# Optimization experiments

Hardware: AMD Instinct MI355X
Metric: run time of the kernel (lower is better)

Reference implementation:

```python
import jax, jax.numpy as jnp
import numpy as np

N_NODES = 50000


def _gcn_conv(h, src, dst, W, b, n_nodes):
    """PyG GCNConv: add self-loops, symmetric deg^{-1/2} normalization,
    linear transform, scatter-add aggregation at target nodes."""
    h = h @ W  # [N, out]
    # self-loops
    loop = jnp.arange(n_nodes, dtype=src.dtype)
    s = jnp.concatenate([src, loop])  # source j
    d = jnp.concatenate([dst, loop])  # target i
    ones = jnp.ones(s.shape[0], dtype=h.dtype)
    deg = jax.ops.segment_sum(ones, d, num_segments=n_nodes)  # in-degree incl. self-loop
    dinv = jnp.where(deg > 0, jax.lax.rsqrt(deg), 0.0)
    norm = dinv[s] * dinv[d]  # [E+N]
    msg = h[s] * norm[:, None]  # gather + scale, [E+N, out]
    out = jax.ops.segment_sum(msg, d, num_segments=n_nodes)  # scatter-add
    return out + b


def reference(x, edge_index, q_emb, W1, b1, W2, b2, Wq, bq):
    src, dst = edge_index[0], edge_index[1]
    n = x.shape[0]
    # dropout rates are 0.0 -> identity
    h1 = jax.nn.relu(_gcn_conv(x, src, dst, W1, b1, n))
    h2 = _gcn_conv(h1, src, dst, W2, b2, n)
    ques = q_emb @ Wq + bq
    return (ques, h2)


def setup_inputs() -> dict:
    key = jax.random.key(0)
    ks = jax.random.split(key, 9)
    d = 128
    sc = 1.0 / np.sqrt(d)
    return {
        "x": jax.random.normal(ks[0], (N_NODES, d), dtype=jnp.float32),
        "edge_index": jax.random.randint(ks[1], (2, 800000), 0, N_NODES, dtype=jnp.int64),
        "q_emb": jax.random.normal(ks[2], (20000, d), dtype=jnp.float32),
        "W1": jax.random.normal(ks[3], (d, d), dtype=jnp.float32) * sc,
        "b1": jax.random.normal(ks[4], (d,), dtype=jnp.float32) * 0.01,
        "W2": jax.random.normal(ks[5], (d, d), dtype=jnp.float32) * sc,
        "b2": jax.random.normal(ks[6], (d,), dtype=jnp.float32) * 0.01,
        "Wq": jax.random.normal(ks[7], (d, d), dtype=jnp.float32) * sc,
        "bq": jax.random.normal(ks[8], (d,), dtype=jnp.float32) * 0.01,
    }
```

## Files before the change

### kernel.cpp

```cpp
#include <hip/hip_runtime.h>

#define D 128
#define NFB 768
#define CAP 64

typedef __attribute__((ext_vector_type(8))) short bf16x8;
typedef __attribute__((ext_vector_type(4))) float f32x4;

__device__ __forceinline__ unsigned short f2b(float v) {
    unsigned u = __float_as_uint(v);
    unsigned r = u + 0x7fffu + ((u >> 16) & 1u);
    return (unsigned short)(r >> 16);
}
__device__ __forceinline__ float b2f(unsigned short h) {
    return __uint_as_float(((unsigned)h) << 16);
}

__global__ __launch_bounds__(256) void fillw(const int* __restrict__ src,
                                             const int* __restrict__ dst,
                                             int* __restrict__ cnt,
                                             int* __restrict__ colv, int E,
                                             const float* __restrict__ W1,
                                             const float* __restrict__ W2,
                                             const float* __restrict__ Wq,
                                             unsigned short* __restrict__ o1,
                                             unsigned short* __restrict__ o2,
                                             unsigned short* __restrict__ oq) {
    int b = blockIdx.x;
    if (b >= NFB) {
        int t = (b - NFB) * 256 + threadIdx.x;
        int which = t >> 14;
        int r = t & 16383;
        int n = r >> 7, k = r & 127;
        const float* W = (which == 0) ? W1 : (which == 1) ? W2 : Wq;
        unsigned short* o = (which == 0) ? o1 : (which == 1) ? o2 : oq;
        o[r] = f2b(W[k * D + n]);
        return;
    }
    const int4* d4 = (const int4*)dst;
    const int4* s4 = (const int4*)src;
    int n4 = E >> 2;
    int stride = NFB * 256;
    for (int idx = b * 256 + threadIdx.x; idx < n4; idx += stride) {
        int4 dv = d4[idx];
        int4 sv = s4[idx];
        int slot;
        slot = atomicAdd(&cnt[dv.x], 1);
        if (slot < CAP) colv[(size_t)dv.x * CAP + slot] = sv.x;
        slot = atomicAdd(&cnt[dv.y], 1);
        if (slot < CAP) colv[(size_t)dv.y * CAP + slot] = sv.y;
        slot = atomicAdd(&cnt[dv.z], 1);
        if (slot < CAP) colv[(size_t)dv.z * CAP + slot] = sv.z;
        slot = atomicAdd(&cnt[dv.w], 1);
        if (slot < CAP) colv[(size_t)dv.w * CAP + slot] = sv.w;
    }
    for (int e = (n4 << 2) + b * 256 + threadIdx.x; e < E; e += stride) {
        int d = dst[e];
        int slot = atomicAdd(&cnt[d], 1);
        if (slot < CAP) colv[(size_t)d * CAP + slot] = src[e];
    }
}


__device__ __forceinline__ void gemm_body(const float* Af,
                                          const unsigned short* __restrict__ Wth,
                                          const float* bias, unsigned short* Cb,
                                          float* Cf, int M, int bid, int outf,
                                          char* smem) {
    int lane = threadIdx.x & 63;
    int wave = threadIdx.x >> 6;
    int m16 = (bid * 4 + wave) * 16;
    if (m16 >= M) return;
    int mrow = lane & 15;
    int quad = lane >> 4;

    f32x4 acc[8];
#pragma unroll
    for (int nt = 0; nt < 8; ++nt) acc[nt] = (f32x4){0.f, 0.f, 0.f, 0.f};

    int arow = m16 + mrow;

#pragma unroll
    for (int ks = 0; ks < 4; ++ks) {
        bf16x8 ah, al;
        const float* ap = Af + (size_t)arow * D + ks * 32 + quad * 8;
        float4 v0 = *(const float4*)ap;
        float4 v1 = *(const float4*)(ap + 4);
        float vv[8] = {v0.x, v0.y, v0.z, v0.w, v1.x, v1.y, v1.z, v1.w};
#pragma unroll
        for (int j = 0; j < 8; ++j) {
            unsigned short h = f2b(vv[j]);
            ah[j] = (short)h;
            al[j] = (short)f2b(vv[j] - b2f(h));
        }
#pragma unroll
        for (int nt = 0; nt < 8; ++nt) {
            bf16x8 wf = *(const bf16x8*)(Wth + (size_t)(nt * 16 + mrow) * D + ks * 32 + quad * 8);
            acc[nt] = __builtin_amdgcn_mfma_f32_16x16x32_bf16(ah, wf, acc[nt], 0, 0, 0);
            acc[nt] = __builtin_amdgcn_mfma_f32_16x16x32_bf16(al, wf, acc[nt], 0, 0, 0);
        }
    }

    if (outf == 0) {
        unsigned short* myl = (unsigned short*)smem + wave * 16 * 136;
#pragma unroll
        for (int nt = 0; nt < 8; ++nt) {
            int col = nt * 16 + mrow;
#pragma unroll
            for (int r = 0; r < 4; ++r)
                myl[(quad * 4 + r) * 136 + col] = f2b(acc[nt][r]);
        }
#pragma unroll
        for (int R = 0; R < 16; ++R) {
            unsigned int v = *(const unsigned int*)&myl[R * 136 + lane * 2];
            ((unsigned int*)(Cb + (size_t)(m16 + R) * D))[lane] = v;
        }
    } else {
#pragma unroll
        for (int nt = 0; nt < 8; ++nt) {
            int col = nt * 16 + mrow;
            float bv = bias[col];
#pragma unroll
            for (int r = 0; r < 4; ++r)
                Cf[(size_t)(m16 + quad * 4 + r) * D + col] = acc[nt][r] + bv;
        }
    }
}

__global__ __launch_bounds__(256) void gemm1q(const float* __restrict__ x,
                                              const float* __restrict__ q,
                                              const unsigned short* __restrict__ Wth1,
                                              const unsigned short* __restrict__ Wthq,
                                              const float* __restrict__ bq,
                                              unsigned short* __restrict__ Cb,
                                              float* __restrict__ outq,
                                              int N, int MQ, int nbN) {
    __shared__ char smem[4 * 16 * 136 * 2];
    int b = blockIdx.x;
    if (b < nbN)
        gemm_body(x, Wth1, nullptr, Cb, nullptr, N, b, 0, smem);
    else
        gemm_body(q, Wthq, bq, nullptr, outq, MQ, b - nbN, 1, smem);
}

__device__ __forceinline__ void agg_node(const bf16x8* __restrict__ T8,
                                         const int* __restrict__ colv,
                                         const int* __restrict__ cnt,
                                         int i, int ci, int lane, int g, int l16,
                                         float acc[8]) {
#pragma unroll
    for (int k = 0; k < 8; ++k) acc[k] = 0.f;
    int jv = 0;
    float wv = 0.f;
    if (lane < ci) {
        jv = colv[i * CAP + lane];
        wv = rsqrtf((float)(cnt[jv] + 1));
    }
    int t = 0;
    for (; t + 16 <= ci; t += 16) {
        int j0 = __shfl(jv, t + g);
        int j1 = __shfl(jv, t + 4 + g);
        int j2 = __shfl(jv, t + 8 + g);
        int j3 = __shfl(jv, t + 12 + g);
        float w0 = __shfl(wv, t + g);
        float w1 = __shfl(wv, t + 4 + g);
        float w2 = __shfl(wv, t + 8 + g);
        float w3 = __shfl(wv, t + 12 + g);
        bf16x8 r0 = T8[(size_t)j0 * 16 + l16];
        bf16x8 r1 = T8[(size_t)j1 * 16 + l16];
        bf16x8 r2 = T8[(size_t)j2 * 16 + l16];
        bf16x8 r3 = T8[(size_t)j3 * 16 + l16];
#pragma unroll
        for (int k = 0; k < 8; ++k) acc[k] = fmaf(w0, b2f((unsigned short)r0[k]), acc[k]);
#pragma unroll
        for (int k = 0; k < 8; ++k) acc[k] = fmaf(w1, b2f((unsigned short)r1[k]), acc[k]);
#pragma unroll
        for (int k = 0; k < 8; ++k) acc[k] = fmaf(w2, b2f((unsigned short)r2[k]), acc[k]);
#pragma unroll
        for (int k = 0; k < 8; ++k) acc[k] = fmaf(w3, b2f((unsigned short)r3[k]), acc[k]);
    }
    for (; t < ci; t += 4) {
        int j = __shfl(jv, t + g);
        float w = __shfl(wv, t + g);
        if (w > 0.f) {
            bf16x8 r = T8[(size_t)j * 16 + l16];
#pragma unroll
            for (int k = 0; k < 8; ++k) acc[k] = fmaf(w, b2f((unsigned short)r[k]), acc[k]);
        }
    }
#pragma unroll
    for (int k = 0; k < 8; ++k) {
        acc[k] += __shfl_xor(acc[k], 16);
        acc[k] += __shfl_xor(acc[k], 32);
    }
}

__global__ __launch_bounds__(512) void agg1_gemm(const unsigned short* __restrict__ Tb,
                                                 const int* __restrict__ colv,
                                                 const int* __restrict__ cnt,
                                                 const float* __restrict__ bias,
                                                 const unsigned short* __restrict__ Wth2,
                                                 unsigned short* __restrict__ Cb2,
                                                 int N) {
    __shared__ unsigned short AH[16 * 136];
    __shared__ unsigned short AL[16 * 136];
    int wave = threadIdx.x >> 6;
    int lane = threadIdx.x & 63;
    int g = lane >> 4;
    int l16 = lane & 15;
    int node0 = blockIdx.x * 16;
    const bf16x8* T8 = (const bf16x8*)Tb;

#pragma unroll
    for (int sub = 0; sub < 2; ++sub) {
        int row = wave * 2 + sub;
        int i = node0 + row;
        float acc[8];
        if (i < N) {
            int deg = cnt[i];
            int ci = (deg < CAP) ? deg : CAP;
            agg_node(T8, colv, cnt, i, ci, lane, g, l16, acc);
            if (g == 0) {
                float di = rsqrtf((float)(deg + 1));
                bf16x8 selfr = T8[(size_t)i * 16 + l16];
                float4 b0 = ((const float4*)bias)[l16 * 2];
                float4 b1v = ((const float4*)bias)[l16 * 2 + 1];
                float bb[8] = {b0.x, b0.y, b0.z, b0.w, b1v.x, b1v.y, b1v.z, b1v.w};
                bf16x8 h, l;
#pragma unroll
                for (int k = 0; k < 8; ++k) {
                    float r = di * acc[k] + di * di * b2f((unsigned short)selfr[k]) + bb[k];
                    r = fmaxf(r, 0.f);
                    unsigned short hh = f2b(r);
                    h[k] = (short)hh;
                    l[k] = (short)f2b(r - b2f(hh));
                }
                *(bf16x8*)&AH[row * 136 + l16 * 8] = h;
                *(bf16x8*)&AL[row * 136 + l16 * 8] = l;
            }
        } else if (g == 0) {
            bf16x8 z = (bf16x8){0, 0, 0, 0, 0, 0, 0, 0};
            *(bf16x8*)&AH[row * 136 + l16 * 8] = z;
            *(bf16x8*)&AL[row * 136 + l16 * 8] = z;
        }
    }
    __syncthreads();

    int nt = wave;
    int mrow = l16;
    int quad = g;
    f32x4 acc2 = (f32x4){0.f, 0.f, 0.f, 0.f};
#pragma unroll
    for (int ks = 0; ks < 4; ++ks) {
        bf16x8 ah = *(const bf16x8*)&AH[mrow * 136 + ks * 32 + quad * 8];
        bf16x8 al = *(const bf16x8*)&AL[mrow * 136 + ks * 32 + quad * 8];
        bf16x8 wf = *(const bf16x8*)(Wth2 + (size_t)(nt * 16 + mrow) * D + ks * 32 + quad * 8);
        acc2 = __builtin_amdgcn_mfma_f32_16x16x32_bf16(ah, wf, acc2, 0, 0, 0);
        acc2 = __builtin_amdgcn_mfma_f32_16x16x32_bf16(al, wf, acc2, 0, 0, 0);
    }
    __syncthreads();
    {
        int col = nt * 16 + mrow;
#pragma unroll
        for (int r = 0; r < 4; ++r) {
            int gi = node0 + quad * 4 + r;
            float dr = (gi < N) ? rsqrtf((float)(cnt[gi] + 1)) : 0.f;
            AH[(quad * 4 + r) * 136 + col] = f2b(acc2[r] * dr);
        }
    }
    __syncthreads();
#pragma unroll
    for (int k = 0; k < 2; ++k) {
        int idx = threadIdx.x + k * 512;
        int row = idx >> 6;
        int c = idx & 63;
        if (node0 + row < N) {
            unsigned int v = *(const unsigned int*)&AH[row * 136 + c * 2];
            ((unsigned int*)(Cb2 + (size_t)(node0 + row) * D))[c] = v;
        }
    }
}

__global__ __launch_bounds__(512) void aggregate2(const unsigned short* __restrict__ Tb,
                                                  const int* __restrict__ colv,
                                                  const int* __restrict__ cnt,
                                                  const float* __restrict__ bias,
                                                  float* __restrict__ Of, int N) {
    int wave = threadIdx.x >> 6;
    int lane = threadIdx.x & 63;
    int i = blockIdx.x * 8 + wave;
    if (i >= N) return;
    int g = lane >> 4;
    int l16 = lane & 15;
    const bf16x8* T8 = (const bf16x8*)Tb;

    int deg = cnt[i];
    int ci = (deg < CAP) ? deg : CAP;
    bf16x8 selfr = T8[(size_t)i * 16 + l16];
    float4 b0 = ((const float4*)bias)[l16 * 2];
    float4 b1v = ((const float4*)bias)[l16 * 2 + 1];

    float acc[8];
#pragma unroll
    for (int k = 0; k < 8; ++k) acc[k] = 0.f;

    int jv = (lane < ci) ? colv[i * CAP + lane] : 0;
    int t = 0;
    for (; t + 16 <= ci; t += 16) {
        int j0 = __shfl(jv, t + g);
        int j1 = __shfl(jv, t + 4 + g);
        int j2 = __shfl(jv, t + 8 + g);
        int j3 = __shfl(jv, t + 12 + g);
        bf16x8 r0 = T8[(size_t)j0 * 16 + l16];
        bf16x8 r1 = T8[(size_t)j1 * 16 + l16];
        bf16x8 r2 = T8[(size_t)j2 * 16 + l16];
        bf16x8 r3 = T8[(size_t)j3 * 16 + l16];
#pragma unroll
        for (int k = 0; k < 8; ++k)
            acc[k] += b2f((unsigned short)r0[k]) + b2f((unsigned short)r1[k]) +
                      b2f((unsigned short)r2[k]) + b2f((unsigned short)r3[k]);
    }
    for (; t < ci; t += 4) {
        int j = __shfl(jv, t + g);
        if (t + g < ci) {
            bf16x8 r = T8[(size_t)j * 16 + l16];
#pragma unroll
            for (int k = 0; k < 8; ++k) acc[k] += b2f((unsigned short)r[k]);
        }
    }

#pragma unroll
    for (int k = 0; k < 8; ++k) {
        acc[k] += __shfl_xor(acc[k], 16);
        acc[k] += __shfl_xor(acc[k], 32);
    }

    if (g == 0) {
        float di = rsqrtf((float)(deg + 1));
        float bb[8] = {b0.x, b0.y, b0.z, b0.w, b1v.x, b1v.y, b1v.z, b1v.w};
        float4 r0, r1;
        r0.x = di * (acc[0] + b2f((unsigned short)selfr[0])) + bb[0];
        r0.y = di * (acc[1] + b2f((unsigned short)selfr[1])) + bb[1];
        r0.z = di * (acc[2] + b2f((unsigned short)selfr[2])) + bb[2];
        r0.w = di * (acc[3] + b2f((unsigned short)selfr[3])) + bb[3];
        r1.x = di * (acc[4] + b2f((unsigned short)selfr[4])) + bb[4];
        r1.y = di * (acc[5] + b2f((unsigned short)selfr[5])) + bb[5];
        r1.z = di * (acc[6] + b2f((unsigned short)selfr[6])) + bb[6];
        r1.w = di * (acc[7] + b2f((unsigned short)selfr[7])) + bb[7];
        ((float4*)Of)[(size_t)i * 32 + l16 * 2] = r0;
        ((float4*)Of)[(size_t)i * 32 + l16 * 2 + 1] = r1;
    }
}


static inline char* carve(char*& w, size_t bytes) {
    char* p = w;
    w += (bytes + 255) & ~(size_t)255;
    return p;
}

extern "C" void kernel_launch(void* const* d_in, const int* in_sizes, int n_in,
                              void* d_out, int out_size, void* d_ws, size_t ws_size,
                              hipStream_t stream) {
    const float* x  = (const float*)d_in[0];
    const int*   ei = (const int*)d_in[1];
    const float* q  = (const float*)d_in[2];
    const float* W1 = (const float*)d_in[3];
    const float* b1 = (const float*)d_in[4];
    const float* W2 = (const float*)d_in[5];
    const float* b2 = (const float*)d_in[6];
    const float* Wq = (const float*)d_in[7];
    const float* bq = (const float*)d_in[8];

    int N  = in_sizes[0] / D;
    int E  = in_sizes[1] / 2;
    int MQ = in_sizes[2] / D;

    const int* srcv = ei;
    const int* dstv = ei + E;

    char* w = (char*)d_ws;
    unsigned short* Cb   = (unsigned short*)carve(w, (size_t)N * D * 2);
    unsigned short* Cb2  = (unsigned short*)carve(w, (size_t)N * D * 2);
    int*            colv = (int*)carve(w, (size_t)N * CAP * 4);
    int*            cnt  = (int*)carve(w, (size_t)N * 4);
    unsigned short* Wth1 = (unsigned short*)carve(w, D * D * 2);
    unsigned short* Wth2 = (unsigned short*)carve(w, D * D * 2);
    unsigned short* Wthq = (unsigned short*)carve(w, D * D * 2);

    float* outq = (float*)d_out;
    float* outh = outq + (size_t)MQ * D;

    int nbN = (N + 63) / 64;
    int nbQ = (MQ + 63) / 64;

    hipMemsetAsync(cnt, 0, (size_t)N * 4, stream);
    fillw<<<NFB + 192, 256, 0, stream>>>(srcv, dstv, cnt, colv, E,
                                         W1, W2, Wq, Wth1, Wth2, Wthq);
    gemm1q<<<nbN + nbQ, 256, 0, stream>>>(x, q, Wth1, Wthq, bq, Cb, outq, N, MQ, nbN);
    agg1_gemm<<<(N + 15) / 16, 512, 0, stream>>>(Cb, colv, cnt, b1, Wth2, Cb2, N);
    aggregate2<<<(N + 7) / 8, 512, 0, stream>>>(Cb2, colv, cnt, b2, outh, N);
}
```

Baseline: 249.6 us.

## Fuse CSR fill with first GEMM and convert weights inline

Merges the edge-bucketing kernel and the x/q GEMM kernel into one launch: the first 256 blocks build the adjacency lists while the remaining blocks run the GEMMs concurrently. The separate weight transpose/bf16 pre-pass is dropped. Each GEMM now reads fp32 weights with a strided column access and converts them to bf16 in registers. This removes a kernel launch and the workspace weight copies. In exchange, every wave redundantly converts weights through strided uncoalesced loads, and the fill now runs on fewer blocks.

Measured after the change: 227.4 us. 8.9% less time.

```diff
diff --git a/kernel.cpp b/kernel.cpp
--- a/kernel.cpp
+++ b/kernel.cpp
@@ -1,7 +1,7 @@
 #include <hip/hip_runtime.h>
 
 #define D 128
-#define NFB 768
+#define NFB 256
 #define CAP 64
 
 typedef __attribute__((ext_vector_type(8))) short bf16x8;
@@ -16,54 +16,9 @@
     return __uint_as_float(((unsigned)h) << 16);
 }
 
-__global__ __launch_bounds__(256) void fillw(const int* __restrict__ src,
-                                             const int* __restrict__ dst,
-                                             int* __restrict__ cnt,
-                                             int* __restrict__ colv, int E,
-                                             const float* __restrict__ W1,
-                                             const float* __restrict__ W2,
-                                             const float* __restrict__ Wq,
-                                             unsigned short* __restrict__ o1,
-                                             unsigned short* __restrict__ o2,
-                                             unsigned short* __restrict__ oq) {
-    int b = blockIdx.x;
-    if (b >= NFB) {
-        int t = (b - NFB) * 256 + threadIdx.x;
-        int which = t >> 14;
-        int r = t & 16383;
-        int n = r >> 7, k = r & 127;
-        const float* W = (which == 0) ? W1 : (which == 1) ? W2 : Wq;
-        unsigned short* o = (which == 0) ? o1 : (which == 1) ? o2 : oq;
-        o[r] = f2b(W[k * D + n]);
-        return;
-    }
-    const int4* d4 = (const int4*)dst;
-    const int4* s4 = (const int4*)src;
-    int n4 = E >> 2;
-    int stride = NFB * 256;
-    for (int idx = b * 256 + threadIdx.x; idx < n4; idx += stride) {
-        int4 dv = d4[idx];
-        int4 sv = s4[idx];
-        int slot;
-        slot = atomicAdd(&cnt[dv.x], 1);
-        if (slot < CAP) colv[(size_t)dv.x * CAP + slot] = sv.x;
-        slot = atomicAdd(&cnt[dv.y], 1);
-        if (slot < CAP) colv[(size_t)dv.y * CAP + slot] = sv.y;
-        slot = atomicAdd(&cnt[dv.z], 1);
-        if (slot < CAP) colv[(size_t)dv.z * CAP + slot] = sv.z;
-        slot = atomicAdd(&cnt[dv.w], 1);
-        if (slot < CAP) colv[(size_t)dv.w * CAP + slot] = sv.w;
-    }
-    for (int e = (n4 << 2) + b * 256 + threadIdx.x; e < E; e += stride) {
-        int d = dst[e];
-        int slot = atomicAdd(&cnt[d], 1);
-        if (slot < CAP) colv[(size_t)d * CAP + slot] = src[e];
-    }
-}
-
 
 __device__ __forceinline__ void gemm_body(const float* Af,
-                                          const unsigned short* __restrict__ Wth,
+                                          const float* __restrict__ W,
                                           const float* bias, unsigned short* Cb,
                                           float* Cf, int M, int bid, int outf,
                                           char* smem) {
@@ -95,7 +50,10 @@
         }
 #pragma unroll
         for (int nt = 0; nt < 8; ++nt) {
-            bf16x8 wf = *(const bf16x8*)(Wth + (size_t)(nt * 16 + mrow) * D + ks * 32 + quad * 8);
+            const float* wp = W + (size_t)(ks * 32 + quad * 8) * D + nt * 16 + mrow;
+            bf16x8 wf;
+#pragma unroll
+            for (int j = 0; j < 8; ++j) wf[j] = (short)f2b(wp[j * D]);
             acc[nt] = __builtin_amdgcn_mfma_f32_16x16x32_bf16(ah, wf, acc[nt], 0, 0, 0);
             acc[nt] = __builtin_amdgcn_mfma_f32_16x16x32_bf16(al, wf, acc[nt], 0, 0, 0);
         }
@@ -127,20 +85,50 @@
     }
 }
 
-__global__ __launch_bounds__(256) void gemm1q(const float* __restrict__ x,
-                                              const float* __restrict__ q,
-                                              const unsigned short* __restrict__ Wth1,
-                                              const unsigned short* __restrict__ Wthq,
-                                              const float* __restrict__ bq,
-                                              unsigned short* __restrict__ Cb,
-                                              float* __restrict__ outq,
-                                              int N, int MQ, int nbN) {
+__global__ __launch_bounds__(256) void frontfill(const float* __restrict__ x,
+                                                 const float* __restrict__ q,
+                                                 const float* __restrict__ W1,
+                                                 const float* __restrict__ Wq,
+                                                 const float* __restrict__ bq,
+                                                 unsigned short* __restrict__ Cb,
+                                                 float* __restrict__ outq,
+                                                 const int* __restrict__ src,
+                                                 const int* __restrict__ dst,
+                                                 int* __restrict__ cnt,
+                                                 int* __restrict__ colv,
+                                                 int N, int MQ, int E, int nbN) {
     __shared__ char smem[4 * 16 * 136 * 2];
     int b = blockIdx.x;
+    if (b < NFB) {
+        const int4* d4 = (const int4*)dst;
+        const int4* s4 = (const int4*)src;
+        int n4 = E >> 2;
+        int stride = NFB * 256;
+        for (int idx = b * 256 + threadIdx.x; idx < n4; idx += stride) {
+            int4 dv = d4[idx];
+            int4 sv = s4[idx];
+            int slot;
+            slot = atomicAdd(&cnt[dv.x], 1);
+            if (slot < CAP) colv[(size_t)dv.x * CAP + slot] = sv.x;
+            slot = atomicAdd(&cnt[dv.y], 1);
+            if (slot < CAP) colv[(size_t)dv.y * CAP + slot] = sv.y;
+            slot = atomicAdd(&cnt[dv.z], 1);
+            if (slot < CAP) colv[(size_t)dv.z * CAP + slot] = sv.z;
+            slot = atomicAdd(&cnt[dv.w], 1);
+            if (slot < CAP) colv[(size_t)dv.w * CAP + slot] = sv.w;
+        }
+        for (int e = (n4 << 2) + b * 256 + threadIdx.x; e < E; e += stride) {
+            int d = dst[e];
+            int slot = atomicAdd(&cnt[d], 1);
+            if (slot < CAP) colv[(size_t)d * CAP + slot] = src[e];
+        }
+        return;
+    }
+    b -= NFB;
     if (b < nbN)
-        gemm_body(x, Wth1, nullptr, Cb, nullptr, N, b, 0, smem);
+        gemm_body(x, W1, nullptr, Cb, nullptr, N, b, 0, smem);
     else
-        gemm_body(q, Wthq, bq, nullptr, outq, MQ, b - nbN, 1, smem);
+        gemm_body(q, Wq, bq, nullptr, outq, MQ, b - nbN, 1, smem);
 }
 
 __device__ __forceinline__ void agg_node(const bf16x8* __restrict__ T8,
@@ -199,7 +187,7 @@
                                                  const int* __restrict__ colv,
                                                  const int* __restrict__ cnt,
                                                  const float* __restrict__ bias,
-                                                 const unsigned short* __restrict__ Wth2,
+                                                 const float* __restrict__ W2,
                                                  unsigned short* __restrict__ Cb2,
                                                  int N) {
     __shared__ unsigned short AH[16 * 136];
@@ -254,7 +242,10 @@
     for (int ks = 0; ks < 4; ++ks) {
         bf16x8 ah = *(const bf16x8*)&AH[mrow * 136 + ks * 32 + quad * 8];
         bf16x8 al = *(const bf16x8*)&AL[mrow * 136 + ks * 32 + quad * 8];
-        bf16x8 wf = *(const bf16x8*)(Wth2 + (size_t)(nt * 16 + mrow) * D + ks * 32 + quad * 8);
+        const float* wp = W2 + (size_t)(ks * 32 + quad * 8) * D + nt * 16 + mrow;
+        bf16x8 wf;
+#pragma unroll
+        for (int j = 0; j < 8; ++j) wf[j] = (short)f2b(wp[j * D]);
         acc2 = __builtin_amdgcn_mfma_f32_16x16x32_bf16(ah, wf, acc2, 0, 0, 0);
         acc2 = __builtin_amdgcn_mfma_f32_16x16x32_bf16(al, wf, acc2, 0, 0, 0);
     }
@@ -384,9 +375,6 @@
     unsigned short* Cb2  = (unsigned short*)carve(w, (size_t)N * D * 2);
     int*            colv = (int*)carve(w, (size_t)N * CAP * 4);
     int*            cnt  = (int*)carve(w, (size_t)N * 4);
-    unsigned short* Wth1 = (unsigned short*)carve(w, D * D * 2);
-    unsigned short* Wth2 = (unsigned short*)carve(w, D * D * 2);
-    unsigned short* Wthq = (unsigned short*)carve(w, D * D * 2);
 
     float* outq = (float*)d_out;
     float* outh = outq + (size_t)MQ * D;
@@ -395,9 +383,9 @@
     int nbQ = (MQ + 63) / 64;
 
     hipMemsetAsync(cnt, 0, (size_t)N * 4, stream);
-    fillw<<<NFB + 192, 256, 0, stream>>>(srcv, dstv, cnt, colv, E,
-                                         W1, W2, Wq, Wth1, Wth2, Wthq);
-    gemm1q<<<nbN + nbQ, 256, 0, stream>>>(x, q, Wth1, Wthq, bq, Cb, outq, N, MQ, nbN);
-    agg1_gemm<<<(N + 15) / 16, 512, 0, stream>>>(Cb, colv, cnt, b1, Wth2, Cb2, N);
+    frontfill<<<NFB + nbN + nbQ, 256, 0, stream>>>(x, q, W1, Wq, bq, Cb, outq,
+                                                   srcv, dstv, cnt, colv,
+                                                   N, MQ, E, nbN);
+    agg1_gemm<<<(N + 15) / 16, 512, 0, stream>>>(Cb, colv, cnt, b1, W2, Cb2, N);
     aggregate2<<<(N + 7) / 8, 512, 0, stream>>>(Cb2, colv, cnt, b2, outh, N);
 }
```
